# Kernel optimization log

Measured on AMD Instinct MI355X. Metric: run time of the kernel, lower is better.

Reference implementation:

```python
import jax, jax.numpy as jnp
import numpy as np

N, K, C = 10000, 64, 128


def setup_inputs() -> dict:
    key = jax.random.key(0)
    ks = jax.random.split(key, 6)
    return {
        "real": jax.random.normal(ks[0], (N, C), dtype=jnp.float32),
        "imag": jax.random.normal(ks[1], (N, C), dtype=jnp.float32),
        "Qreal": jax.random.normal(ks[2], (N, K), dtype=jnp.float32) / np.sqrt(N),
        "Qimag": jax.random.normal(ks[3], (N, K), dtype=jnp.float32) / np.sqrt(N),
        "Ritz": jax.random.uniform(ks[4], (K,), dtype=jnp.float32),
        "weight": jax.random.normal(ks[5], (C, C), dtype=jnp.float32) * np.sqrt(2.0 / (C + C)),  # xavier-ish scale
        "long_diff": 5,
    }


def reference(real, imag, Qreal, Qimag, Ritz, weight, long_diff):
    # TT = Ritz ** long_diff ; spectral filters L = Q diag(TT) Q^H split into real/imag
    TT = jnp.power(Ritz, long_diff)  # [K]
    QrT = Qreal * TT  # [N,K] columns scaled by TT (== Qreal @ diag(TT))
    QiT = Qimag * TT
    L_real = QrT @ Qreal.T + QiT @ Qimag.T  # [N,N]
    L_imag = QiT @ Qreal.T - QrT @ Qimag.T  # [N,N]
    # complex spmm + shared dense weight: (L @ X_complex) @ W
    res_real = (L_real @ real - L_imag @ imag) @ weight  # [N,C]
    res_imag = (L_imag @ real + L_real @ imag) @ weight  # [N,C]
    # complex ReLU: mask by sign of real part
    mask = (res_real >= 0).astype(res_real.dtype)
    return real + mask * res_real, imag + mask * res_imag
```

## Files before the change

### kernel.cpp

```cpp
#include <hip/hip_runtime.h>

#define NN 10000
#define KK 64
#define CC 128
#define OUTOFF (NN * CC)
#define ROWS 20
#define NCH 500
#define PART_F4 4096

#define ROW_OFF  ((size_t)NCH * 16384)
#define UVW_OFF  (ROW_OFF + 16384)

__device__ __forceinline__ float4 f4fma(float s, float4 v, float4 a) {
    a.x = fmaf(s, v.x, a.x); a.y = fmaf(s, v.y, a.y);
    a.z = fmaf(s, v.z, a.z); a.w = fmaf(s, v.w, a.w);
    return a;
}
__device__ __forceinline__ float4 f4add(float4 a, float4 b) {
    a.x += b.x; a.y += b.y; a.z += b.z; a.w += b.w; return a;
}

__global__ __launch_bounds__(256) void kA(const float* __restrict__ re,
                                          const float* __restrict__ im,
                                          const float* __restrict__ Qr,
                                          const float* __restrict__ Qi,
                                          float* __restrict__ part)
{
    __shared__ float4 smem[1920];
    const int t = threadIdx.x;
    const int bid = blockIdx.x;
    {
        const float4* gqr = (const float4*)Qr;
        const float4* gqi = (const float4*)Qi;
        const float4* gre = (const float4*)re;
        const float4* gim = (const float4*)im;
        for (int i = t; i < 1920; i += 256) {
            float4 v;
            if (i < 320)       v = gqr[(size_t)bid * 320 + i];
            else if (i < 640)  v = gqi[(size_t)bid * 320 + (i - 320)];
            else if (i < 1280) v = gre[(size_t)bid * 640 + (i - 640)];
            else               v = gim[(size_t)bid * 640 + (i - 1280)];
            smem[i] = v;
        }
    }
    __syncthreads();
    const int kt = t >> 4;
    const int c8 = t & 15;
    float aU[4][8] = {}, aV[4][8] = {};
#pragma unroll 4
    for (int rr = 0; rr < ROWS; ++rr) {
        float4 q_r = smem[rr * 16 + kt];
        float4 q_i = smem[320 + rr * 16 + kt];
        float4 x_r0 = smem[640 + rr * 32 + c8 * 2];
        float4 x_r1 = smem[640 + rr * 32 + c8 * 2 + 1];
        float4 x_i0 = smem[1280 + rr * 32 + c8 * 2];
        float4 x_i1 = smem[1280 + rr * 32 + c8 * 2 + 1];
        float qr_[4] = {q_r.x, q_r.y, q_r.z, q_r.w};
        float qi_[4] = {q_i.x, q_i.y, q_i.z, q_i.w};
        float xr_[8] = {x_r0.x, x_r0.y, x_r0.z, x_r0.w, x_r1.x, x_r1.y, x_r1.z, x_r1.w};
        float xi_[8] = {x_i0.x, x_i0.y, x_i0.z, x_i0.w, x_i1.x, x_i1.y, x_i1.z, x_i1.w};
#pragma unroll
        for (int a = 0; a < 4; ++a)
#pragma unroll
            for (int b = 0; b < 8; ++b) {
                aU[a][b] = fmaf(qr_[a], xr_[b], aU[a][b]);
                aU[a][b] = fmaf(qi_[a], xi_[b], aU[a][b]);
                aV[a][b] = fmaf(qi_[a], xr_[b], aV[a][b]);
                aV[a][b] = fmaf(-qr_[a], xi_[b], aV[a][b]);
            }
    }
    float* base = part + (size_t)bid * 16384;
    const int k0 = kt * 4, c0 = c8 * 8;
#pragma unroll
    for (int a = 0; a < 4; ++a) {
        *(float4*)(base + (k0 + a) * CC + c0)            = make_float4(aU[a][0], aU[a][1], aU[a][2], aU[a][3]);
        *(float4*)(base + (k0 + a) * CC + c0 + 4)        = make_float4(aU[a][4], aU[a][5], aU[a][6], aU[a][7]);
        *(float4*)(base + 8192 + (k0 + a) * CC + c0)     = make_float4(aV[a][0], aV[a][1], aV[a][2], aV[a][3]);
        *(float4*)(base + 8192 + (k0 + a) * CC + c0 + 4) = make_float4(aV[a][4], aV[a][5], aV[a][6], aV[a][7]);
    }
}

__global__ __launch_bounds__(512) void kR1(const float* __restrict__ part,
                                           float* __restrict__ row)
{
    __shared__ float4 red4[512];
    const int t = threadIdx.x;
    const int i = t & 15;
    const int g = t >> 4;
    const int o = blockIdx.x * 16 + i;
    const float4* p = (const float4*)part + (size_t)g * PART_F4 + o;
    const float4 z = make_float4(0.f, 0.f, 0.f, 0.f);
    float4 s0 = z, s1 = z, s2 = z, s3 = z;
    int pp = g;
    for (; pp + 96 < NCH; pp += 128) {
        s0 = f4add(s0, p[0]);
        s1 = f4add(s1, p[(size_t)32 * PART_F4]);
        s2 = f4add(s2, p[(size_t)64 * PART_F4]);
        s3 = f4add(s3, p[(size_t)96 * PART_F4]);
        p += (size_t)128 * PART_F4;
    }
    for (; pp < NCH; pp += 32) {
        s0 = f4add(s0, p[0]);
        p += (size_t)32 * PART_F4;
    }
    red4[t] = f4add(f4add(s0, s1), f4add(s2, s3));
    __syncthreads();
    if (t < 16) {
        float4 tot = z;
#pragma unroll
        for (int gg = 0; gg < 32; ++gg) tot = f4add(tot, red4[gg * 16 + t]);
        ((float4*)row)[blockIdx.x * 16 + t] = tot;
    }
}

__global__ __launch_bounds__(128) void kR2(const float* __restrict__ row,
                                           const float* __restrict__ Ritz,
                                           const int* __restrict__ ldp,
                                           const float* __restrict__ W,
                                           float* __restrict__ UVW)
{
    __shared__ float rowS[128];
    const int t = threadIdx.x;
    const int m = blockIdx.x >> 6, k = blockIdx.x & 63;
    rowS[t] = row[m * 8192 + k * 128 + t];
    __syncthreads();
    float acc = 0.f;
#pragma unroll 8
    for (int cp = 0; cp < 128; ++cp)
        acc = fmaf(rowS[cp], W[cp * 128 + t], acc);
    const int ld = *ldp;
    const float rz = Ritz[k];
    float tt = 1.f;
    for (int i = 0; i < ld; ++i) tt *= rz;
    UVW[m * 8192 + k * 128 + t] = tt * acc;
}

__global__ __launch_bounds__(128) void kC(const float* __restrict__ re,
                                          const float* __restrict__ im,
                                          const float* __restrict__ Qr,
                                          const float* __restrict__ Qi,
                                          const float* __restrict__ UVW,
                                          float* __restrict__ out)
{
    const int t = threadIdx.x;
    const int ct = t & 31;
    const int rq = t >> 5;
    const int r0 = blockIdx.x * 16 + rq * 4;
    const float4* U4 = (const float4*)UVW;
    const float4* V4 = U4 + 2048;
    const float4* qr0 = (const float4*)(Qr + (size_t)r0 * KK);
    const float4* qi0 = (const float4*)(Qi + (size_t)r0 * KK);

    const float4 z = make_float4(0.f, 0.f, 0.f, 0.f);
    float4 R[4] = {z, z, z, z}, I[4] = {z, z, z, z};

#pragma unroll 4
    for (int k4 = 0; k4 < 16; ++k4) {
        float4 qr[4], qi[4];
#pragma unroll
        for (int j = 0; j < 4; ++j) {
            qr[j] = qr0[j * 16 + k4];
            qi[j] = qi0[j * 16 + k4];
        }
#pragma unroll
        for (int jj = 0; jj < 4; ++jj) {
            const int k = k4 * 4 + jj;
            float4 uw = U4[k * 32 + ct];
            float4 vw = V4[k * 32 + ct];
#pragma unroll
            for (int j = 0; j < 4; ++j) {
                float ar[4] = {qr[j].x, qr[j].y, qr[j].z, qr[j].w};
                float ai[4] = {qi[j].x, qi[j].y, qi[j].z, qi[j].w};
                R[j] = f4fma(ar[jj], uw, R[j]); R[j] = f4fma(ai[jj], vw, R[j]);
                I[j] = f4fma(ai[jj], uw, I[j]); I[j] = f4fma(-ar[jj], vw, I[j]);
            }
        }
    }
    const int cc = ct * 4;
#pragma unroll
    for (int j = 0; j < 4; ++j) {
        const int row = r0 + j;
        float4 rin = *(const float4*)(re + (size_t)row * CC + cc);
        float4 iin = *(const float4*)(im + (size_t)row * CC + cc);
        float4 orr, oii;
        orr.x = rin.x + (R[j].x >= 0.f ? R[j].x : 0.f); oii.x = iin.x + (R[j].x >= 0.f ? I[j].x : 0.f);
        orr.y = rin.y + (R[j].y >= 0.f ? R[j].y : 0.f); oii.y = iin.y + (R[j].y >= 0.f ? I[j].y : 0.f);
        orr.z = rin.z + (R[j].z >= 0.f ? R[j].z : 0.f); oii.z = iin.z + (R[j].z >= 0.f ? I[j].z : 0.f);
        orr.w = rin.w + (R[j].w >= 0.f ? R[j].w : 0.f); oii.w = iin.w + (R[j].w >= 0.f ? I[j].w : 0.f);
        *(float4*)(out + (size_t)row * CC + cc)          = orr;
        *(float4*)(out + OUTOFF + (size_t)row * CC + cc) = oii;
    }
}

extern "C" void kernel_launch(void* const* d_in, const int* in_sizes, int n_in,
                              void* d_out, int out_size, void* d_ws, size_t ws_size,
                              hipStream_t stream) {
    const float* re   = (const float*)d_in[0];
    const float* im   = (const float*)d_in[1];
    const float* Qr   = (const float*)d_in[2];
    const float* Qi   = (const float*)d_in[3];
    const float* Ritz = (const float*)d_in[4];
    const float* W    = (const float*)d_in[5];
    const int*   ldp  = (const int*)d_in[6];
    float* out = (float*)d_out;
    float* ws  = (float*)d_ws;

    float* part = ws;
    float* row  = ws + ROW_OFF;
    float* UVW  = ws + UVW_OFF;

    kA <<<NCH, 256, 0, stream>>>(re, im, Qr, Qi, part);
    kR1<<<256, 512, 0, stream>>>(part, row);
    kR2<<<128, 128, 0, stream>>>(row, Ritz, ldp, W, UVW);
    kC <<<625, 128, 0, stream>>>(re, im, Qr, Qi, UVW, out);
}
```

Measured before the change: 126.1 us.

## Fuse partial reduction with weight matmul and split K across threads in output kernel

Merges the two reduction kernels into one 1024-thread kernel per (m,k) row that sums the chunk partials and applies the weight matrix and Ritz power. The separate row buffer and one launch go away. The first kernel now uses 625 chunks of 16 rows. The output kernel doubles its threads and splits the K loop in two halves, combining them through shared memory, which adds parallelism at the cost of a barrier and more partial data to reduce.

Result: faster. 122.1 us (-3.1%).

```diff
diff --git a/kernel.cpp b/kernel.cpp
--- a/kernel.cpp
+++ b/kernel.cpp
@@ -4,12 +4,11 @@
 #define KK 64
 #define CC 128
 #define OUTOFF (NN * CC)
-#define ROWS 20
-#define NCH 500
+#define ROWS 16
+#define NCH 625
 #define PART_F4 4096
 
-#define ROW_OFF  ((size_t)NCH * 16384)
-#define UVW_OFF  (ROW_OFF + 16384)
+#define UVW_OFF  ((size_t)NCH * 16384)
 
 __device__ __forceinline__ float4 f4fma(float s, float4 v, float4 a) {
     a.x = fmaf(s, v.x, a.x); a.y = fmaf(s, v.y, a.y);
@@ -26,7 +25,7 @@
                                           const float* __restrict__ Qi,
                                           float* __restrict__ part)
 {
-    __shared__ float4 smem[1920];
+    __shared__ float4 smem[1536];
     const int t = threadIdx.x;
     const int bid = blockIdx.x;
     {
@@ -34,12 +33,12 @@
         const float4* gqi = (const float4*)Qi;
         const float4* gre = (const float4*)re;
         const float4* gim = (const float4*)im;
-        for (int i = t; i < 1920; i += 256) {
+        for (int i = t; i < 1536; i += 256) {
             float4 v;
-            if (i < 320)       v = gqr[(size_t)bid * 320 + i];
-            else if (i < 640)  v = gqi[(size_t)bid * 320 + (i - 320)];
-            else if (i < 1280) v = gre[(size_t)bid * 640 + (i - 640)];
-            else               v = gim[(size_t)bid * 640 + (i - 1280)];
+            if (i < 256)       v = gqr[(size_t)bid * 256 + i];
+            else if (i < 512)  v = gqi[(size_t)bid * 256 + (i - 256)];
+            else if (i < 1024) v = gre[(size_t)bid * 512 + (i - 512)];
+            else               v = gim[(size_t)bid * 512 + (i - 1024)];
             smem[i] = v;
         }
     }
@@ -50,11 +49,11 @@
 #pragma unroll 4
     for (int rr = 0; rr < ROWS; ++rr) {
         float4 q_r = smem[rr * 16 + kt];
-        float4 q_i = smem[320 + rr * 16 + kt];
-        float4 x_r0 = smem[640 + rr * 32 + c8 * 2];
-        float4 x_r1 = smem[640 + rr * 32 + c8 * 2 + 1];
-        float4 x_i0 = smem[1280 + rr * 32 + c8 * 2];
-        float4 x_i1 = smem[1280 + rr * 32 + c8 * 2 + 1];
+        float4 q_i = smem[256 + rr * 16 + kt];
+        float4 x_r0 = smem[512 + rr * 32 + c8 * 2];
+        float4 x_r1 = smem[512 + rr * 32 + c8 * 2 + 1];
+        float4 x_i0 = smem[1024 + rr * 32 + c8 * 2];
+        float4 x_i1 = smem[1024 + rr * 32 + c8 * 2 + 1];
         float qr_[4] = {q_r.x, q_r.y, q_r.z, q_r.w};
         float qi_[4] = {q_i.x, q_i.y, q_i.z, q_i.w};
         float xr_[8] = {x_r0.x, x_r0.y, x_r0.z, x_r0.w, x_r1.x, x_r1.y, x_r1.z, x_r1.w};
@@ -80,72 +79,62 @@
     }
 }
 
-__global__ __launch_bounds__(512) void kR1(const float* __restrict__ part,
-                                           float* __restrict__ row)
+__global__ __launch_bounds__(1024) void kRB(const float* __restrict__ part,
+                                            const float* __restrict__ Ritz,
+                                            const int* __restrict__ ldp,
+                                            const float* __restrict__ W,
+                                            float* __restrict__ UVW)
 {
-    __shared__ float4 red4[512];
-    const int t = threadIdx.x;
-    const int i = t & 15;
-    const int g = t >> 4;
-    const int o = blockIdx.x * 16 + i;
-    const float4* p = (const float4*)part + (size_t)g * PART_F4 + o;
-    const float4 z = make_float4(0.f, 0.f, 0.f, 0.f);
-    float4 s0 = z, s1 = z, s2 = z, s3 = z;
-    int pp = g;
-    for (; pp + 96 < NCH; pp += 128) {
-        s0 = f4add(s0, p[0]);
-        s1 = f4add(s1, p[(size_t)32 * PART_F4]);
-        s2 = f4add(s2, p[(size_t)64 * PART_F4]);
-        s3 = f4add(s3, p[(size_t)96 * PART_F4]);
-        p += (size_t)128 * PART_F4;
-    }
-    for (; pp < NCH; pp += 32) {
-        s0 = f4add(s0, p[0]);
-        p += (size_t)32 * PART_F4;
-    }
-    red4[t] = f4add(f4add(s0, s1), f4add(s2, s3));
-    __syncthreads();
-    if (t < 16) {
-        float4 tot = z;
-#pragma unroll
-        for (int gg = 0; gg < 32; ++gg) tot = f4add(tot, red4[gg * 16 + t]);
-        ((float4*)row)[blockIdx.x * 16 + t] = tot;
-    }
-}
-
-__global__ __launch_bounds__(128) void kR2(const float* __restrict__ row,
-                                           const float* __restrict__ Ritz,
-                                           const int* __restrict__ ldp,
-                                           const float* __restrict__ W,
-                                           float* __restrict__ UVW)
-{
-    __shared__ float rowS[128];
+    __shared__ float4 red4[1024];
+    __shared__ float  rowS[128];
     const int t = threadIdx.x;
     const int m = blockIdx.x >> 6, k = blockIdx.x & 63;
-    rowS[t] = row[m * 8192 + k * 128 + t];
-    __syncthreads();
-    float acc = 0.f;
+    const int q = t & 31, d = t >> 5;
+    const float4* p0 = (const float4*)part + (size_t)m * 2048 + k * 32 + q;
+    const float4 z = make_float4(0.f, 0.f, 0.f, 0.f);
+    float4 s0 = z, s1 = z;
+    int pp = d;
+    for (; pp + 32 < NCH; pp += 64) {
+        s0 = f4add(s0, p0[(size_t)pp * PART_F4]);
+        s1 = f4add(s1, p0[(size_t)(pp + 32) * PART_F4]);
+    }
+    if (pp < NCH) s0 = f4add(s0, p0[(size_t)pp * PART_F4]);
+    red4[t] = f4add(s0, s1);
+    __syncthreads();
+    if (t < 32) {
+        float4 tot = z;
+#pragma unroll
+        for (int dd = 0; dd < 32; ++dd) tot = f4add(tot, red4[dd * 32 + t]);
+        ((float4*)rowS)[t] = tot;
+    }
+    __syncthreads();
+    if (t < 128) {
+        float acc = 0.f;
 #pragma unroll 8
-    for (int cp = 0; cp < 128; ++cp)
-        acc = fmaf(rowS[cp], W[cp * 128 + t], acc);
-    const int ld = *ldp;
-    const float rz = Ritz[k];
-    float tt = 1.f;
-    for (int i = 0; i < ld; ++i) tt *= rz;
-    UVW[m * 8192 + k * 128 + t] = tt * acc;
-}
-
-__global__ __launch_bounds__(128) void kC(const float* __restrict__ re,
+        for (int cp = 0; cp < 128; ++cp)
+            acc = fmaf(rowS[cp], W[cp * 128 + t], acc);
+        const int ld = *ldp;
+        const float rz = Ritz[k];
+        float tt = 1.f;
+        for (int i = 0; i < ld; ++i) tt *= rz;
+        UVW[m * 8192 + k * 128 + t] = tt * acc;
+    }
+}
+
+__global__ __launch_bounds__(256) void kC(const float* __restrict__ re,
                                           const float* __restrict__ im,
                                           const float* __restrict__ Qr,
                                           const float* __restrict__ Qi,
                                           const float* __restrict__ UVW,
                                           float* __restrict__ out)
 {
+    __shared__ float4 xch[1024];
     const int t = threadIdx.x;
     const int ct = t & 31;
-    const int rq = t >> 5;
+    const int rq = (t >> 5) & 3;
+    const int kh = t >> 7;
     const int r0 = blockIdx.x * 16 + rq * 4;
+    const int idx = rq * 32 + ct;
     const float4* U4 = (const float4*)UVW;
     const float4* V4 = U4 + 2048;
     const float4* qr0 = (const float4*)(Qr + (size_t)r0 * KK);
@@ -154,8 +143,9 @@
     const float4 z = make_float4(0.f, 0.f, 0.f, 0.f);
     float4 R[4] = {z, z, z, z}, I[4] = {z, z, z, z};
 
-#pragma unroll 4
-    for (int k4 = 0; k4 < 16; ++k4) {
+    const int k4lo = kh * 8;
+#pragma unroll
+    for (int k4 = k4lo; k4 < k4lo + 8; ++k4) {
         float4 qr[4], qi[4];
 #pragma unroll
         for (int j = 0; j < 4; ++j) {
@@ -176,19 +166,34 @@
             }
         }
     }
-    const int cc = ct * 4;
-#pragma unroll
-    for (int j = 0; j < 4; ++j) {
-        const int row = r0 + j;
-        float4 rin = *(const float4*)(re + (size_t)row * CC + cc);
-        float4 iin = *(const float4*)(im + (size_t)row * CC + cc);
-        float4 orr, oii;
-        orr.x = rin.x + (R[j].x >= 0.f ? R[j].x : 0.f); oii.x = iin.x + (R[j].x >= 0.f ? I[j].x : 0.f);
-        orr.y = rin.y + (R[j].y >= 0.f ? R[j].y : 0.f); oii.y = iin.y + (R[j].y >= 0.f ? I[j].y : 0.f);
-        orr.z = rin.z + (R[j].z >= 0.f ? R[j].z : 0.f); oii.z = iin.z + (R[j].z >= 0.f ? I[j].z : 0.f);
-        orr.w = rin.w + (R[j].w >= 0.f ? R[j].w : 0.f); oii.w = iin.w + (R[j].w >= 0.f ? I[j].w : 0.f);
-        *(float4*)(out + (size_t)row * CC + cc)          = orr;
-        *(float4*)(out + OUTOFF + (size_t)row * CC + cc) = oii;
+    if (kh == 1) {
+#pragma unroll
+        for (int j = 0; j < 4; ++j) {
+            xch[j * 128 + idx]       = R[j];
+            xch[(4 + j) * 128 + idx] = I[j];
+        }
+    }
+    __syncthreads();
+    if (kh == 0) {
+#pragma unroll
+        for (int j = 0; j < 4; ++j) {
+            R[j] = f4add(R[j], xch[j * 128 + idx]);
+            I[j] = f4add(I[j], xch[(4 + j) * 128 + idx]);
+        }
+        const int cc = ct * 4;
+#pragma unroll
+        for (int j = 0; j < 4; ++j) {
+            const int row = r0 + j;
+            float4 rin = *(const float4*)(re + (size_t)row * CC + cc);
+            float4 iin = *(const float4*)(im + (size_t)row * CC + cc);
+            float4 orr, oii;
+            orr.x = rin.x + (R[j].x >= 0.f ? R[j].x : 0.f); oii.x = iin.x + (R[j].x >= 0.f ? I[j].x : 0.f);
+            orr.y = rin.y + (R[j].y >= 0.f ? R[j].y : 0.f); oii.y = iin.y + (R[j].y >= 0.f ? I[j].y : 0.f);
+            orr.z = rin.z + (R[j].z >= 0.f ? R[j].z : 0.f); oii.z = iin.z + (R[j].z >= 0.f ? I[j].z : 0.f);
+            orr.w = rin.w + (R[j].w >= 0.f ? R[j].w : 0.f); oii.w = iin.w + (R[j].w >= 0.f ? I[j].w : 0.f);
+            *(float4*)(out + (size_t)row * CC + cc)          = orr;
+            *(float4*)(out + OUTOFF + (size_t)row * CC + cc) = oii;
+        }
     }
 }
 
@@ -206,11 +211,9 @@
     float* ws  = (float*)d_ws;
 
     float* part = ws;
-    float* row  = ws + ROW_OFF;
     float* UVW  = ws + UVW_OFF;
 
-    kA <<<NCH, 256, 0, stream>>>(re, im, Qr, Qi, part);
-    kR1<<<256, 512, 0, stream>>>(part, row);
-    kR2<<<128, 128, 0, stream>>>(row, Ritz, ldp, W, UVW);
-    kC <<<625, 128, 0, stream>>>(re, im, Qr, Qi, UVW, out);
-}
+    kA <<<NCH, 256,  0, stream>>>(re, im, Qr, Qi, part);
+    kRB<<<128, 1024, 0, stream>>>(part, Ritz, ldp, W, UVW);
+    kC <<<NCH, 256,  0, stream>>>(re, im, Qr, Qi, UVW, out);
+}
```
